# Kernel tuning notes

Hardware: AMD Instinct MI355X
Metric: run time of the kernel (lower is better)

## Reference

```python
import jax, jax.numpy as jnp
import numpy as np

N = 50000        # nodes
E = 800000       # directed edges (before self loops)
G = 1024         # graphs in batch
D = 128          # embedding_dim
H = 4            # attention heads
L = 3            # num_layers
NODE_DIM = 78
SLOPE = 0.2      # PyG GATConv leaky_relu negative slope
EPS = 1e-16


def setup_inputs() -> dict:
    key = jax.random.key(0)
    ks = jax.random.split(key, 20)
    s = lambda *sh: 1.0 / np.sqrt(sh[0])
    inp = {
        "x": jax.random.normal(ks[0], (N, NODE_DIM), jnp.float32),
        "edge_index": jax.random.randint(ks[1], (2, E), 0, N, jnp.int64),
        "batch": jnp.sort(jax.random.randint(ks[2], (N,), 0, G, jnp.int64)),
        # node_linear: Linear(78,128) -> ReLU -> Linear(128,128)
        "W1": jax.random.normal(ks[3], (NODE_DIM, D), jnp.float32) * s(NODE_DIM),
        "b1": jnp.zeros((D,), jnp.float32),
        "W2": jax.random.normal(ks[4], (D, D), jnp.float32) * s(D),
        "b2": jnp.zeros((D,), jnp.float32),
        # L stacked GATConv(D, D, heads=H, concat=False)
        "lin_w": jax.random.normal(ks[5], (L, D, H, D), jnp.float32) * s(D),
        "att_src": jax.random.normal(ks[6], (L, H, D), jnp.float32) * s(D),
        "att_dst": jax.random.normal(ks[7], (L, H, D), jnp.float32) * s(D),
        "conv_b": jnp.zeros((L, D), jnp.float32),
        # global_fc: Linear(128,1024) -> ReLU -> Dropout -> Linear(1024,128)
        "gW1": jax.random.normal(ks[8], (D, 1024), jnp.float32) * s(D),
        "gb1": jnp.zeros((1024,), jnp.float32),
        "gW2": jax.random.normal(ks[9], (1024, D), jnp.float32) * s(1024),
        "gb2": jnp.zeros((D,), jnp.float32),
    }
    return inp


def _gat_layer(x, src, dst, W, a_src, a_dst, b):
    # x: [N, D]; W: [D, H, D]
    h = jnp.einsum('nd,dhe->nhe', x, W)                    # [N, H, C]
    a_s = jnp.einsum('nhe,he->nh', h, a_src)               # [N, H]
    a_d = jnp.einsum('nhe,he->nh', h, a_dst)
    e = jax.nn.leaky_relu(a_s[src] + a_d[dst], SLOPE)      # [E', H]
    # segment softmax grouped by destination node
    m = jax.ops.segment_max(e, dst, num_segments=N)
    e = jnp.exp(e - m[dst])
    denom = jax.ops.segment_sum(e, dst, num_segments=N)
    alpha = e / (denom[dst] + EPS)                         # [E', H]
    out = jax.ops.segment_sum(h[src] * alpha[:, :, None], dst, num_segments=N)  # [N, H, C]
    return out.mean(axis=1) + b                            # concat=False: head mean


def reference(x, edge_index, batch, W1, b1, W2, b2, lin_w, att_src, att_dst,
              conv_b, gW1, gb1, gW2, gb2):
    # node_linear MLP
    h = jax.nn.relu(x @ W1 + b1) @ W2 + b2                 # [N, D]
    # add self loops (PyG GATConv default)
    loops = jnp.arange(N, dtype=edge_index.dtype)
    src = jnp.concatenate([edge_index[0], loops])
    dst = jnp.concatenate([edge_index[1], loops])
    for l in range(L):
        h = _gat_layer(h, src, dst, lin_w[l], att_src[l], att_dst[l], conv_b[l])
    # global mean pool per graph
    counts = jax.ops.segment_sum(jnp.ones((N,), h.dtype), batch, num_segments=G)
    pooled = jax.ops.segment_sum(h, batch, num_segments=G) / jnp.maximum(counts, 1.0)[:, None]
    # global_fc (dropout = identity at inference)
    return jax.nn.relu(pooled @ gW1 + gb1) @ gW2 + gb2     # [G, D]
```

## Files before the change

kernel.cpp:

```cpp
#include <hip/hip_runtime.h>
#include <hip/hip_bf16.h>

#define NN 50000
#define EE 800000
#define ET 850000
#define GG 1024
#define DD 128
#define HH 4
#define LL 3
#define ND 78
#define HD 512
#define K1P 96
#define SLOPE 0.2f
#define EPSV 1e-16f
#define SB 196
#define PADS 520

typedef __hip_bfloat16 bf16;
typedef __attribute__((ext_vector_type(8))) unsigned short u16x8;
typedef __attribute__((ext_vector_type(8))) short s16x8;
typedef __attribute__((ext_vector_type(4))) float f32x4;
typedef __attribute__((ext_vector_type(2))) float f32x2;

__device__ __forceinline__ float b2f(bf16 v) { return __bfloat162float(v); }
__device__ __forceinline__ bf16 f2b(float v) { return __float2bfloat16(v); }
__device__ __forceinline__ float bu2f(unsigned short u) {
    return __uint_as_float(((unsigned)u) << 16);
}
__device__ __forceinline__ unsigned short f2bu(float f) {
    unsigned u = __float_as_uint(f);
    unsigned rounded = u + 0x7FFFu + ((u >> 16) & 1u);
    return (unsigned short)(rounded >> 16);
}
__device__ __forceinline__ float lrelu(float e) { return (e > 0.f) ? e : SLOPE * e; }

__global__ void detect_i(const unsigned* __restrict__ w, int* __restrict__ flag) {
    __shared__ int z;
    int t = threadIdx.x;
    if (t == 0) z = 0;
    __syncthreads();
    if (w[2 * t + 1] == 0u) atomicAdd(&z, 1);
    __syncthreads();
    if (t == 0) flag[0] = (z >= 200) ? 1 : 0;
}
__global__ void conv_i(const void* __restrict__ src, int* __restrict__ dst, int n,
                       const int* __restrict__ flag) {
    int i = blockIdx.x * 256 + threadIdx.x;
    if (i >= n) return;
    const int* s = (const int*)src;
    dst[i] = flag[0] ? s[2 * i] : s[i];
}
__global__ void conv_edges(const void* __restrict__ src, int* __restrict__ dst,
                           const int* __restrict__ flag, int* __restrict__ deg) {
    int i = blockIdx.x * 256 + threadIdx.x;
    if (i < NN) deg[i] = 1;
    if (i >= 2 * EE) return;
    const int* s = (const int*)src;
    dst[i] = flag[0] ? s[2 * i] : s[i];
}

#define PRE0 (NN * K1P)
#define PRE1 (PRE0 + DD * K1P + DD * DD)
#define PRE2 (PRE1 + LL * DD * HD)
#define PRE3 (PRE2 + 2 * 1024 * DD)
#define PRE4 (PRE3 + LL * DD * HH)
#define PRE5 (PRE4 + GG * DD + GG)
__global__ void prep_misc(const float* __restrict__ x, const float* __restrict__ W1,
                          const float* __restrict__ W2, const float* __restrict__ lin_w,
                          const float* __restrict__ att_src, const float* __restrict__ att_dst,
                          const float* __restrict__ gW1, const float* __restrict__ gW2,
                          bf16* __restrict__ xb, bf16* __restrict__ W1t, bf16* __restrict__ W2t,
                          bf16* __restrict__ Bt, float* __restrict__ ws, float* __restrict__ wd,
                          bf16* __restrict__ gW1t, bf16* __restrict__ gW2t,
                          float* __restrict__ pooled, int* __restrict__ counts) {
    int idx = blockIdx.x * 256 + threadIdx.x;
    if (idx < PRE0) {
        int n = idx / K1P;
        int k = idx % K1P;
        xb[idx] = f2b((k < ND) ? x[(size_t)n * ND + k] : 0.f);
        return;
    }
    if (idx < PRE1) {
        idx -= PRE0;
        if (idx < DD * K1P) {
            int c = idx / K1P, k = idx % K1P;
            W1t[idx] = f2b((k < ND) ? W1[(size_t)k * DD + c] : 0.f);
        } else {
            idx -= DD * K1P;
            int c = idx / DD, k = idx % DD;
            W2t[idx] = f2b(W2[(size_t)k * DD + c]);
        }
        return;
    }
    if (idx < PRE2) {
        idx -= PRE1;
        int l = idx / (DD * HD);
        int rem = idx % (DD * HD);
        int c = rem / HD;
        int k = rem % HD;
        int h = k >> 7;
        int d = k & 127;
        Bt[idx] = f2b(lin_w[((size_t)(l * DD + d) * HH + h) * DD + c]);
        return;
    }
    if (idx < PRE3) {
        idx -= PRE2;
        if (idx < 1024 * DD) {
            int c = idx / DD, k = idx % DD;
            gW1t[idx] = f2b(gW1[(size_t)k * 1024 + c]);
        } else {
            idx -= 1024 * DD;
            int c = idx / 1024, k = idx % 1024;
            gW2t[idx] = f2b(gW2[(size_t)k * DD + c]);
        }
        return;
    }
    if (idx < PRE4) {
        idx -= PRE3;
        int l = idx / (DD * HH);
        int rem = idx % (DD * HH);
        int d = rem >> 2;
        int h = rem & 3;
        const float* wrow = lin_w + ((size_t)(l * DD + d) * HH + h) * DD;
        const float* as = att_src + (size_t)(l * HH + h) * DD;
        const float* ad = att_dst + (size_t)(l * HH + h) * DD;
        float s1 = 0.f, s2 = 0.f;
        for (int e = 0; e < DD; e++) { float w = wrow[e]; s1 += w * as[e]; s2 += w * ad[e]; }
        ws[idx] = s1;
        wd[idx] = s2;
        return;
    }
    if (idx < PRE5) {
        idx -= PRE4;
        if (idx < GG * DD) pooled[idx] = 0.f;
        if (idx < GG) counts[idx] = 0;
    }
}

__global__ __launch_bounds__(256) void mlp_gemm1(const bf16* __restrict__ xb,
                                                 const bf16* __restrict__ W1t,
                                                 const float* __restrict__ b1,
                                                 bf16* __restrict__ ts) {
    int wid = (blockIdx.x * 256 + threadIdx.x) >> 6;
    if (wid >= NN / 16) return;
    int lane = threadIdx.x & 63;
    int r16 = lane & 15;
    int q = lane >> 4;
    const short* ab = (const short*)xb;
    const short* bb = (const short*)W1t;
    int arow = wid * 16 + r16;
    s16x8 afr[3];
#pragma unroll
    for (int c = 0; c < 3; c++) afr[c] = *(const s16x8*)(ab + (size_t)arow * K1P + c * 32 + q * 8);
#pragma unroll
    for (int nt = 0; nt < 8; nt++) {
        int brow = nt * 16 + r16;
        f32x4 acc = {0.f, 0.f, 0.f, 0.f};
#pragma unroll
        for (int c = 0; c < 3; c++) {
            s16x8 b = *(const s16x8*)(bb + (size_t)brow * K1P + c * 32 + q * 8);
            acc = __builtin_amdgcn_mfma_f32_16x16x32_bf16(afr[c], b, acc, 0, 0, 0);
        }
        int cc = nt * 16 + r16;
        float bias = b1[cc];
#pragma unroll
        for (int r = 0; r < 4; r++) {
            int row = wid * 16 + q * 4 + r;
            ts[(size_t)row * DD + cc] = f2b(fmaxf(acc[r] + bias, 0.f));
        }
    }
}

__global__ __launch_bounds__(256) void mlp_gemm2(const bf16* __restrict__ ts,
                                                 const bf16* __restrict__ W2t,
                                                 const float* __restrict__ b2,
                                                 bf16* __restrict__ h) {
    int wid = (blockIdx.x * 256 + threadIdx.x) >> 6;
    if (wid >= NN / 16) return;
    int lane = threadIdx.x & 63;
    int r16 = lane & 15;
    int q = lane >> 4;
    const short* ab = (const short*)ts;
    const short* bb = (const short*)W2t;
    int arow = wid * 16 + r16;
    s16x8 afr[4];
#pragma unroll
    for (int c = 0; c < 4; c++) afr[c] = *(const s16x8*)(ab + (size_t)arow * DD + c * 32 + q * 8);
#pragma unroll
    for (int nt = 0; nt < 8; nt++) {
        int brow = nt * 16 + r16;
        f32x4 acc = {0.f, 0.f, 0.f, 0.f};
#pragma unroll
        for (int c = 0; c < 4; c++) {
            s16x8 b = *(const s16x8*)(bb + (size_t)brow * DD + c * 32 + q * 8);
            acc = __builtin_amdgcn_mfma_f32_16x16x32_bf16(afr[c], b, acc, 0, 0, 0);
        }
        int cc = nt * 16 + r16;
        float bias = b2[cc];
#pragma unroll
        for (int r = 0; r < 4; r++) {
            int row = wid * 16 + q * 4 + r;
            h[(size_t)row * DD + cc] = f2b(acc[r] + bias);
        }
    }
}

__global__ void hist_edges(const int* __restrict__ ei, int* deg) {
    int e = blockIdx.x * 256 + threadIdx.x;
    if (e >= EE) return;
    int dst = ei[EE + e];
    if ((unsigned)dst < NN) atomicAdd(&deg[dst], 1);
}
__global__ __launch_bounds__(256) void block_sums(const int* __restrict__ deg, int* __restrict__ bsum) {
    __shared__ int part[256];
    int t = threadIdx.x;
    int i = blockIdx.x * 256 + t;
    part[t] = (i < NN) ? deg[i] : 0;
    __syncthreads();
    for (int off = 128; off > 0; off >>= 1) {
        if (t < off) part[t] += part[t + off];
        __syncthreads();
    }
    if (t == 0) bsum[blockIdx.x] = part[0];
}
__global__ __launch_bounds__(256) void scan_bsum(const int* __restrict__ bsum, int* __restrict__ boff,
                                                 int* __restrict__ start) {
    __shared__ int part[256];
    int t = threadIdx.x;
    part[t] = (t < SB) ? bsum[t] : 0;
    __syncthreads();
    for (int off = 1; off < 256; off <<= 1) {
        int add = (t >= off) ? part[t - off] : 0;
        __syncthreads();
        part[t] += add;
        __syncthreads();
    }
    if (t < SB) boff[t] = (t == 0) ? 0 : part[t - 1];
    if (t == 255) start[NN] = part[SB - 1];
}
__global__ __launch_bounds__(256) void scan_final(const int* __restrict__ deg, const int* __restrict__ boff,
                                                  int* __restrict__ start, int* __restrict__ cursor) {
    __shared__ int part[256];
    int t = threadIdx.x;
    int i = blockIdx.x * 256 + t;
    int v = (i < NN) ? deg[i] : 0;
    part[t] = v;
    __syncthreads();
    for (int off = 1; off < 256; off <<= 1) {
        int add = (t >= off) ? part[t - off] : 0;
        __syncthreads();
        part[t] += add;
        __syncthreads();
    }
    if (i < NN) {
        int ex = boff[blockIdx.x] + part[t] - v;
        start[i] = ex;
        cursor[i] = ex;
    }
}
__global__ void scatter_all(const int* __restrict__ ei, int* cursor, int* ssrc) {
    int i = blockIdx.x * 256 + threadIdx.x;
    if (i < NN) {
        int pos = atomicAdd(&cursor[i], 1);
        if ((unsigned)pos < ET) ssrc[pos] = i;
        return;
    }
    int e = i - NN;
    if (e >= EE) return;
    int src = ei[e];
    int dst = ei[EE + e];
    if ((unsigned)dst >= NN) return;
    int pos = atomicAdd(&cursor[dst], 1);
    if ((unsigned)pos < ET) ssrc[pos] = ((unsigned)src < NN) ? src : 0;
}

__global__ __launch_bounds__(256) void a_sd2(const bf16* __restrict__ h,
                                             const float* __restrict__ ws,
                                             const float* __restrict__ wd,
                                             float* __restrict__ a_s, float* __restrict__ a_d) {
    __shared__ float wsl[DD][HH];
    __shared__ float wdl[DD][HH];
    int t = threadIdx.x;
    for (int i = t; i < DD * HH; i += 256) { wsl[i >> 2][i & 3] = ws[i]; wdl[i >> 2][i & 3] = wd[i]; }
    __syncthreads();
    int n = blockIdx.x * 256 + t;
    if (n >= NN) return;
    const u16x8* row = (const u16x8*)((const unsigned short*)h + (size_t)n * DD);
    float s1[HH] = {0.f, 0.f, 0.f, 0.f};
    float s2[HH] = {0.f, 0.f, 0.f, 0.f};
    for (int c = 0; c < 16; c++) {
        u16x8 v = row[c];
#pragma unroll
        for (int k = 0; k < 8; k++) {
            int d = c * 8 + k;
            float f = bu2f(v[k]);
#pragma unroll
            for (int hh = 0; hh < HH; hh++) {
                s1[hh] += f * wsl[d][hh];
                s2[hh] += f * wdl[d][hh];
            }
        }
    }
#pragma unroll
    for (int hh = 0; hh < HH; hh++) {
        a_s[n * HH + hh] = s1[hh];
        a_d[n * HH + hh] = s2[hh];
    }
}

__global__ __launch_bounds__(1024, 8) void agg_gemm(const int* __restrict__ start,
                                                    const int* __restrict__ ssrc,
                                                    const float* __restrict__ a_s,
                                                    const float* __restrict__ a_d,
                                                    const bf16* __restrict__ h,
                                                    const bf16* __restrict__ Bt,
                                                    const float* __restrict__ conv_b,
                                                    bf16* __restrict__ hnext) {
    __shared__ short aggL[16 * PADS];
    __shared__ float wlds[16][64][HH];
    __shared__ float mxl[16][HH];
    __shared__ float invl[16][HH];
    int wv = threadIdx.x >> 6;
    int lane = threadIdx.x & 63;
    int half = lane >> 5;
    int sl = lane & 31;
    int node16 = blockIdx.x * 16;
    int node = node16 + wv;

    int s0 = start[node];
    int deg = start[node + 1] - s0;
    int sidx = (lane < deg) ? ssrc[s0 + lane] : 0;
    int soff = sidx << 8;

    const char* hb = (const char*)h;
    int lb8 = sl << 3;

    auto issueChunk = [&](int j, uint2 (&hv)[4]) {
#pragma unroll
        for (int p = 0; p < 4; p++) {
            int sa = __builtin_amdgcn_readlane(soff, j + 2 * p);
            int sb = __builtin_amdgcn_readlane(soff, j + 2 * p + 1);
            hv[p] = *(const uint2*)(hb + ((half ? sb : sa) + lb8));
        }
    };

    int m = (deg > 64) ? 64 : deg;
    int nch = (m + 7) >> 3;
    uint2 hva[4], hvb[4];
    issueChunk(0, hva);

    {
        int jj = lane & 15;
        int hh = lane >> 4;
        float ad = a_d[node * HH + hh];
        float ec[4];
        float mx = -1e30f;
#pragma unroll
        for (int k = 0; k < 4; k++) {
            int j = jj + k * 16;
            float e = -1e30f;
            if (j < deg) {
                int s = __shfl(sidx, j);
                e = lrelu(a_s[s * HH + hh] + ad);
            }
            ec[k] = e;
            mx = fmaxf(mx, e);
        }
        for (int j = jj + 64; j < deg; j += 16) {
            int s = ssrc[s0 + j];
            mx = fmaxf(mx, lrelu(a_s[s * HH + hh] + ad));
        }
#pragma unroll
        for (int off = 1; off < 16; off <<= 1) mx = fmaxf(mx, __shfl_xor(mx, off));
        float den = 0.f;
#pragma unroll
        for (int k = 0; k < 4; k++) {
            int j = jj + k * 16;
            float ww = __expf(ec[k] - mx);
            den += ww;
            wlds[wv][j][hh] = ww;
        }
        for (int j = jj + 64; j < deg; j += 16) {
            int s = ssrc[s0 + j];
            den += __expf(lrelu(a_s[s * HH + hh] + ad) - mx);
        }
#pragma unroll
        for (int off = 1; off < 16; off <<= 1) den += __shfl_xor(den, off);
        if (jj == 0) {
            invl[wv][hh] = 1.f / (den + EPSV);
            mxl[wv][hh] = mx;
        }
    }

    f32x2 accA[HH];
    f32x2 accB[HH];
#pragma unroll
    for (int hh = 0; hh < HH; hh++) { accA[hh] = (f32x2){0.f, 0.f}; accB[hh] = (f32x2){0.f, 0.f}; }

    auto consumeChunk = [&](int j, uint2 (&hv)[4]) {
#pragma unroll
        for (int p = 0; p < 4; p++) {
            float4 w4 = *(const float4*)wlds[wv][j + 2 * p + half];
            f32x2 vA, vB;
            vA.x = __uint_as_float(hv[p].x << 16);
            vA.y = __uint_as_float(hv[p].x & 0xffff0000u);
            vB.x = __uint_as_float(hv[p].y << 16);
            vB.y = __uint_as_float(hv[p].y & 0xffff0000u);
            accA[0] += vA * w4.x; accB[0] += vB * w4.x;
            accA[1] += vA * w4.y; accB[1] += vB * w4.y;
            accA[2] += vA * w4.z; accB[2] += vB * w4.z;
            accA[3] += vA * w4.w; accB[3] += vB * w4.w;
        }
    };

    {
        int c = 0;
        for (;;) {
            if (c + 1 < nch) issueChunk((c + 1) * 8, hvb);
            consumeChunk(c * 8, hva);
            if (++c >= nch) break;
            if (c + 1 < nch) issueChunk((c + 1) * 8, hva);
            consumeChunk(c * 8, hvb);
            if (++c >= nch) break;
        }
    }

    for (int j = 64; j < deg; j++) {
        int s = ssrc[s0 + j];
        float4 as4 = *(const float4*)(a_s + (size_t)s * HH);
        float4 ad4 = *(const float4*)(a_d + (size_t)node * HH);
        float4 w4;
        float g = half ? 0.f : 1.f;
        w4.x = g * __expf(lrelu(as4.x + ad4.x) - mxl[wv][0]);
        w4.y = g * __expf(lrelu(as4.y + ad4.y) - mxl[wv][1]);
        w4.z = g * __expf(lrelu(as4.z + ad4.z) - mxl[wv][2]);
        w4.w = g * __expf(lrelu(as4.w + ad4.w) - mxl[wv][3]);
        uint2 hv = *(const uint2*)(hb + ((size_t)s << 8) + lb8);
        f32x2 vA, vB;
        vA.x = __uint_as_float(hv.x << 16);
        vA.y = __uint_as_float(hv.x & 0xffff0000u);
        vB.x = __uint_as_float(hv.y << 16);
        vB.y = __uint_as_float(hv.y & 0xffff0000u);
        accA[0] += vA * w4.x; accB[0] += vB * w4.x;
        accA[1] += vA * w4.y; accB[1] += vB * w4.y;
        accA[2] += vA * w4.z; accB[2] += vB * w4.z;
        accA[3] += vA * w4.w; accB[3] += vB * w4.w;
    }

#pragma unroll
    for (int hh = 0; hh < HH; hh++) {
        accA[hh].x += __shfl_xor(accA[hh].x, 32);
        accA[hh].y += __shfl_xor(accA[hh].y, 32);
        accB[hh].x += __shfl_xor(accB[hh].x, 32);
        accB[hh].y += __shfl_xor(accB[hh].y, 32);
    }

    float4 inv4 = *(const float4*)invl[wv];
    float invs[HH] = {inv4.x, inv4.y, inv4.z, inv4.w};
    unsigned* aggU = (unsigned*)aggL;
#pragma unroll
    for (int hh = 0; hh < HH; hh++) {
        f32x2 sel = half ? accB[hh] : accA[hh];
        unsigned packed = (unsigned)f2bu(sel.x * invs[hh]) |
                          ((unsigned)f2bu(sel.y * invs[hh]) << 16);
        aggU[wv * (PADS / 2) + hh * (DD / 2) + sl * 2 + half] = packed;
    }
    __syncthreads();

    if (wv < 8) {
        int nt = wv;
        int r16 = lane & 15;
        int q = lane >> 4;
        const short* bb = (const short*)Bt;
        int brow = nt * 16 + r16;
        f32x4 gacc = {0.f, 0.f, 0.f, 0.f};
#pragma unroll
        for (int c = 0; c < 16; c++) {
            s16x8 a = *(const s16x8*)(aggL + r16 * PADS + c * 32 + q * 8);
            s16x8 b = *(const s16x8*)(bb + (size_t)brow * HD + c * 32 + q * 8);
            gacc = __builtin_amdgcn_mfma_f32_16x16x32_bf16(a, b, gacc, 0, 0, 0);
        }
        int cc = nt * 16 + r16;
        float bias = conv_b[cc];
#pragma unroll
        for (int r = 0; r < 4; r++) {
            int row = node16 + q * 4 + r;
            hnext[(size_t)row * DD + cc] = f2b(0.25f * gacc[r] + bias);
        }
    }
}

__global__ void pool_count(const int* __restrict__ batch, int* counts) {
    int n = blockIdx.x * 256 + threadIdx.x;
    if (n >= NN) return;
    int g = batch[n];
    if ((unsigned)g < GG) atomicAdd(&counts[g], 1);
}
__global__ __launch_bounds__(256) void pool_accum2(const bf16* __restrict__ h,
                                                   const int* __restrict__ batch,
                                                   float* pooled) {
    int t = threadIdx.x;
    int d = t & 127;
    int half = t >> 7;
    int n0 = blockIdx.x * 64 + half * 32;
    int n1 = n0 + 32; if (n1 > NN) n1 = NN;
    float acc = 0.f;
    int cur = -1;
    for (int n = n0; n < n1; n++) {
        int g = batch[n];
        if ((unsigned)g >= GG) continue;
        if (g != cur) {
            if (cur >= 0) atomicAdd(&pooled[cur * DD + d], acc);
            acc = 0.f; cur = g;
        }
        acc += b2f(h[(size_t)n * DD + d]);
    }
    if (cur >= 0) atomicAdd(&pooled[cur * DD + d], acc);
}
__global__ void pooled2bf(const float* __restrict__ pooled, const int* __restrict__ counts,
                          bf16* __restrict__ pbf) {
    int idx = blockIdx.x * 256 + threadIdx.x;
    if (idx >= GG * DD) return;
    int g = idx >> 7;
    int c = counts[g]; if (c < 1) c = 1;
    pbf[idx] = f2b(pooled[idx] / (float)c);
}

__global__ __launch_bounds__(256) void fc1_mfma(const bf16* __restrict__ pbf,
                                                const bf16* __restrict__ gW1t,
                                                const float* __restrict__ gb1,
                                                bf16* __restrict__ t1) {
    int wid = (blockIdx.x * 256 + threadIdx.x) >> 6;
    int lane = threadIdx.x & 63;
    int mt = wid >> 6;
    int nt = wid & 63;
    int r16 = lane & 15;
    int q = lane >> 4;
    const short* ab = (const short*)pbf;
    const short* bb = (const short*)gW1t;
    f32x4 acc = {0.f, 0.f, 0.f, 0.f};
    int arow = mt * 16 + r16;
    int brow = nt * 16 + r16;
#pragma unroll
    for (int c = 0; c < 4; c++) {
        s16x8 a = *(const s16x8*)(ab + (size_t)arow * DD + c * 32 + q * 8);
        s16x8 b = *(const s16x8*)(bb + (size_t)brow * DD + c * 32 + q * 8);
        acc = __builtin_amdgcn_mfma_f32_16x16x32_bf16(a, b, acc, 0, 0, 0);
    }
    int cc = nt * 16 + r16;
    float bias = gb1[cc];
#pragma unroll
    for (int r = 0; r < 4; r++) {
        int row = mt * 16 + q * 4 + r;
        t1[(size_t)row * 1024 + cc] = f2b(fmaxf(acc[r] + bias, 0.f));
    }
}

__global__ __launch_bounds__(256) void fc2_mfma(const bf16* __restrict__ t1,
                                                const bf16* __restrict__ gW2t,
                                                const float* __restrict__ gb2,
                                                float* __restrict__ out) {
    int wid = (blockIdx.x * 256 + threadIdx.x) >> 6;
    int lane = threadIdx.x & 63;
    int mt = wid >> 3;
    int nt = wid & 7;
    int r16 = lane & 15;
    int q = lane >> 4;
    const short* ab = (const short*)t1;
    const short* bb = (const short*)gW2t;
    f32x4 acc = {0.f, 0.f, 0.f, 0.f};
    int arow = mt * 16 + r16;
    int brow = nt * 16 + r16;
#pragma unroll
    for (int c = 0; c < 32; c++) {
        s16x8 a = *(const s16x8*)(ab + (size_t)arow * 1024 + c * 32 + q * 8);
        s16x8 b = *(const s16x8*)(bb + (size_t)brow * 1024 + c * 32 + q * 8);
        acc = __builtin_amdgcn_mfma_f32_16x16x32_bf16(a, b, acc, 0, 0, 0);
    }
    int cc = nt * 16 + r16;
    float bias = gb2[cc];
#pragma unroll
    for (int r = 0; r < 4; r++) {
        int row = mt * 16 + q * 4 + r;
        out[(size_t)row * DD + cc] = acc[r] + bias;
    }
}

__global__ void sentinel_only(float* out, int hostcode) {
    if (threadIdx.x == 0 && blockIdx.x == 0) out[0] = (float)hostcode;
}

extern "C" void kernel_launch(void* const* d_in, const int* in_sizes, int n_in,
                              void* d_out, int out_size, void* d_ws, size_t ws_size,
                              hipStream_t stream) {
    float* out = (float*)d_out;

    static const int expect[15] = {3900000, 1600000, 50000, 9984, 128, 16384, 128,
                                   196608, 1536, 1536, 384, 131072, 1024, 131072, 128};
    int hostcode = 0;
    if (n_in != 15) hostcode = 21099;
    else for (int i = 0; i < 15; i++) if (in_sizes[i] != expect[i]) { hostcode = 21000 + i; break; }
    if (hostcode == 0 && out_size != GG * DD) hostcode = 35000;

    const float* x       = (const float*)d_in[0];
    const float* W1      = (const float*)d_in[3];
    const float* b1      = (const float*)d_in[4];
    const float* W2      = (const float*)d_in[5];
    const float* b2      = (const float*)d_in[6];
    const float* lin_w   = (const float*)d_in[7];
    const float* att_src = (const float*)d_in[8];
    const float* att_dst = (const float*)d_in[9];
    const float* conv_b  = (const float*)d_in[10];
    const float* gW1     = (const float*)d_in[11];
    const float* gb1     = (const float*)d_in[12];
    const float* gW2     = (const float*)d_in[13];
    const float* gb2     = (const float*)d_in[14];

    char* p = (char*)d_ws;
    auto alloc = [&](size_t bytes) { void* q = (void*)p; p += (bytes + 255) & ~(size_t)255; return q; };
    int*   flags  = (int*)alloc(4 * 4);
    int*   ei32   = (int*)alloc((size_t)2 * EE * 4);
    int*   bat32  = (int*)alloc((size_t)NN * 4);
    bf16*  xb     = (bf16*)alloc((size_t)NN * K1P * 2);
    bf16*  W1tb   = (bf16*)alloc((size_t)DD * K1P * 2);
    bf16*  W2tb   = (bf16*)alloc((size_t)DD * DD * 2);
    bf16*  tsbuf  = (bf16*)alloc((size_t)NN * DD * 2);
    bf16*  hA     = (bf16*)alloc((size_t)NN * DD * 2);
    bf16*  hB     = (bf16*)alloc((size_t)NN * DD * 2);
    bf16*  Bt     = (bf16*)alloc((size_t)LL * DD * HD * 2);
    float* wsbuf  = (float*)alloc((size_t)LL * DD * HH * 4);
    float* wdbuf  = (float*)alloc((size_t)LL * DD * HH * 4);
    float* a_s    = (float*)alloc((size_t)NN * HH * 4);
    float* a_d    = (float*)alloc((size_t)NN * HH * 4);
    int*   deg    = (int*)alloc((size_t)NN * 4);
    int*   start  = (int*)alloc((size_t)(NN + 1) * 4);
    int*   cursor = (int*)alloc((size_t)NN * 4);
    int*   ssrc   = (int*)alloc((size_t)ET * 4);
    int*   bsum   = (int*)alloc((size_t)SB * 4);
    int*   boff   = (int*)alloc((size_t)SB * 4);
    float* pooled = (float*)alloc((size_t)GG * DD * 4);
    int*   counts = (int*)alloc((size_t)GG * 4);
    bf16*  pbf    = (bf16*)alloc((size_t)GG * DD * 2);
    bf16*  gW1t   = (bf16*)alloc((size_t)1024 * DD * 2);
    bf16*  gW2t   = (bf16*)alloc((size_t)DD * 1024 * 2);
    bf16*  t1buf  = (bf16*)alloc((size_t)GG * 1024 * 2);
    size_t need = (size_t)(p - (char*)d_ws);
    if (hostcode == 0 && ws_size < need) hostcode = 34000;

    if (hostcode != 0) {
        sentinel_only<<<1, 64, 0, stream>>>(out, hostcode);
        return;
    }

    detect_i<<<1, 256, 0, stream>>>((const unsigned*)d_in[1], flags + 0);
    detect_i<<<1, 256, 0, stream>>>((const unsigned*)d_in[2], flags + 1);
    conv_edges<<<(2 * EE + 255) / 256, 256, 0, stream>>>(d_in[1], ei32, flags + 0, deg);
    conv_i<<<(NN + 255) / 256, 256, 0, stream>>>(d_in[2], bat32, NN, flags + 1);

    prep_misc<<<PRE5 / 256, 256, 0, stream>>>(x, W1, W2, lin_w, att_src, att_dst, gW1, gW2,
                                              xb, W1tb, W2tb, Bt, wsbuf, wdbuf, gW1t, gW2t,
                                              pooled, counts);

    mlp_gemm1<<<(NN / 16 * 64 + 255) / 256, 256, 0, stream>>>(xb, W1tb, b1, tsbuf);
    mlp_gemm2<<<(NN / 16 * 64 + 255) / 256, 256, 0, stream>>>(tsbuf, W2tb, b2, hA);

    hist_edges<<<(EE + 255) / 256, 256, 0, stream>>>(ei32, deg);
    block_sums<<<SB, 256, 0, stream>>>(deg, bsum);
    scan_bsum<<<1, 256, 0, stream>>>(bsum, boff, start);
    scan_final<<<SB, 256, 0, stream>>>(deg, boff, start, cursor);
    scatter_all<<<(NN + EE + 255) / 256, 256, 0, stream>>>(ei32, cursor, ssrc);

    bf16* hin = hA;
    bf16* hout = hB;
    for (int l = 0; l < LL; l++) {
        a_sd2<<<(NN + 255) / 256, 256, 0, stream>>>(hin, wsbuf + l * DD * HH, wdbuf + l * DD * HH, a_s, a_d);
        agg_gemm<<<NN / 16, 1024, 0, stream>>>(start, ssrc, a_s, a_d, hin,
                                               Bt + (size_t)l * DD * HD, conv_b + l * DD, hout);
        bf16* tmp = hin; hin = hout; hout = tmp;
    }
    pool_count<<<(NN + 255) / 256, 256, 0, stream>>>(bat32, counts);
    pool_accum2<<<(NN + 63) / 64, 256, 0, stream>>>(hin, bat32, pooled);
    pooled2bf<<<(GG * DD + 255) / 256, 256, 0, stream>>>(pooled, counts, pbf);
    fc1_mfma<<<(64 * 64) / 4, 256, 0, stream>>>(pbf, gW1t, gb1, t1buf);
    fc2_mfma<<<(64 * 8) / 4, 256, 0, stream>>>(t1buf, gW2t, gb2, out);
}
```

Baseline: 572.9 us.

## Fuse MLP GEMMs, attention-score epilogues, and preprocessing kernels to cut launches

Merges the two node-MLP GEMMs into one kernel that keeps the hidden tile in LDS, and computes the layer-0 attention scores in its epilogue. Each GAT aggregation kernel now also computes the next layer's a_s/a_d in its epilogue, so the separate a_sd2 pass is gone. Int64 detection, degree histogram and graph counts are folded into the conversion kernels, and the pooled normalization moves into fc1. This removes several launches and full passes over h, at the cost of extra shuffles and an extra block-wide sync in agg_gemm, plus redundant detection work repeated in every block.

```diff
diff --git a/kernel.cpp b/kernel.cpp
--- a/kernel.cpp
+++ b/kernel.cpp
@@ -34,37 +34,13 @@
 }
 __device__ __forceinline__ float lrelu(float e) { return (e > 0.f) ? e : SLOPE * e; }
 
-__global__ void detect_i(const unsigned* __restrict__ w, int* __restrict__ flag) {
-    __shared__ int z;
-    int t = threadIdx.x;
-    if (t == 0) z = 0;
-    __syncthreads();
-    if (w[2 * t + 1] == 0u) atomicAdd(&z, 1);
-    __syncthreads();
-    if (t == 0) flag[0] = (z >= 200) ? 1 : 0;
-}
-__global__ void conv_i(const void* __restrict__ src, int* __restrict__ dst, int n,
-                       const int* __restrict__ flag) {
-    int i = blockIdx.x * 256 + threadIdx.x;
-    if (i >= n) return;
-    const int* s = (const int*)src;
-    dst[i] = flag[0] ? s[2 * i] : s[i];
-}
-__global__ void conv_edges(const void* __restrict__ src, int* __restrict__ dst,
-                           const int* __restrict__ flag, int* __restrict__ deg) {
-    int i = blockIdx.x * 256 + threadIdx.x;
-    if (i < NN) deg[i] = 1;
-    if (i >= 2 * EE) return;
-    const int* s = (const int*)src;
-    dst[i] = flag[0] ? s[2 * i] : s[i];
-}
-
 #define PRE0 (NN * K1P)
 #define PRE1 (PRE0 + DD * K1P + DD * DD)
 #define PRE2 (PRE1 + LL * DD * HD)
 #define PRE3 (PRE2 + 2 * 1024 * DD)
 #define PRE4 (PRE3 + LL * DD * HH)
 #define PRE5 (PRE4 + GG * DD + GG)
+#define PRE6 (PRE5 + NN)
 __global__ void prep_misc(const float* __restrict__ x, const float* __restrict__ W1,
                           const float* __restrict__ W2, const float* __restrict__ lin_w,
                           const float* __restrict__ att_src, const float* __restrict__ att_dst,
@@ -72,7 +48,8 @@
                           bf16* __restrict__ xb, bf16* __restrict__ W1t, bf16* __restrict__ W2t,
                           bf16* __restrict__ Bt, float* __restrict__ ws, float* __restrict__ wd,
                           bf16* __restrict__ gW1t, bf16* __restrict__ gW2t,
-                          float* __restrict__ pooled, int* __restrict__ counts) {
+                          float* __restrict__ pooled, int* __restrict__ counts,
+                          int* __restrict__ deg) {
     int idx = blockIdx.x * 256 + threadIdx.x;
     if (idx < PRE0) {
         int n = idx / K1P;
@@ -134,83 +111,148 @@
         idx -= PRE4;
         if (idx < GG * DD) pooled[idx] = 0.f;
         if (idx < GG) counts[idx] = 0;
-    }
-}
-
-__global__ __launch_bounds__(256) void mlp_gemm1(const bf16* __restrict__ xb,
+        return;
+    }
+    if (idx < PRE6) {
+        deg[idx - PRE5] = 1;
+    }
+}
+
+__global__ void conv_edges(const void* __restrict__ src, int* __restrict__ dst,
+                           int* __restrict__ deg) {
+    __shared__ int z;
+    int t = threadIdx.x;
+    const unsigned* w = (const unsigned*)src;
+    if (t == 0) z = 0;
+    __syncthreads();
+    if (w[2 * t + 1] == 0u) atomicAdd(&z, 1);
+    __syncthreads();
+    int flag = (z >= 200) ? 1 : 0;
+    int i = blockIdx.x * 256 + t;
+    if (i >= 2 * EE) return;
+    const int* s = (const int*)src;
+    int g = flag ? s[2 * i] : s[i];
+    dst[i] = g;
+    if (i >= EE && (unsigned)g < NN) atomicAdd(&deg[g], 1);
+}
+
+__global__ void conv_batch(const void* __restrict__ src, int* __restrict__ dst,
+                           int* __restrict__ counts) {
+    __shared__ int z;
+    int t = threadIdx.x;
+    const unsigned* w = (const unsigned*)src;
+    if (t == 0) z = 0;
+    __syncthreads();
+    if (w[2 * t + 1] == 0u) atomicAdd(&z, 1);
+    __syncthreads();
+    int flag = (z >= 200) ? 1 : 0;
+    int i = blockIdx.x * 256 + t;
+    if (i >= NN) return;
+    const int* s = (const int*)src;
+    int g = flag ? s[2 * i] : s[i];
+    dst[i] = g;
+    if ((unsigned)g < GG) atomicAdd(&counts[g], 1);
+}
+
+__global__ __launch_bounds__(256) void mlp_fused(const bf16* __restrict__ xb,
                                                  const bf16* __restrict__ W1t,
                                                  const float* __restrict__ b1,
-                                                 bf16* __restrict__ ts) {
+                                                 const bf16* __restrict__ W2t,
+                                                 const float* __restrict__ b2,
+                                                 const float* __restrict__ ws0,
+                                                 const float* __restrict__ wd0,
+                                                 bf16* __restrict__ h,
+                                                 float* __restrict__ a_s, float* __restrict__ a_d) {
+    __shared__ __align__(16) short tsl[4][16][136];
+    int wv4 = threadIdx.x >> 6;
     int wid = (blockIdx.x * 256 + threadIdx.x) >> 6;
     if (wid >= NN / 16) return;
     int lane = threadIdx.x & 63;
     int r16 = lane & 15;
     int q = lane >> 4;
-    const short* ab = (const short*)xb;
-    const short* bb = (const short*)W1t;
-    int arow = wid * 16 + r16;
-    s16x8 afr[3];
-#pragma unroll
-    for (int c = 0; c < 3; c++) afr[c] = *(const s16x8*)(ab + (size_t)arow * K1P + c * 32 + q * 8);
-#pragma unroll
-    for (int nt = 0; nt < 8; nt++) {
-        int brow = nt * 16 + r16;
-        f32x4 acc = {0.f, 0.f, 0.f, 0.f};
-#pragma unroll
-        for (int c = 0; c < 3; c++) {
-            s16x8 b = *(const s16x8*)(bb + (size_t)brow * K1P + c * 32 + q * 8);
-            acc = __builtin_amdgcn_mfma_f32_16x16x32_bf16(afr[c], b, acc, 0, 0, 0);
-        }
-        int cc = nt * 16 + r16;
-        float bias = b1[cc];
-#pragma unroll
-        for (int r = 0; r < 4; r++) {
-            int row = wid * 16 + q * 4 + r;
-            ts[(size_t)row * DD + cc] = f2b(fmaxf(acc[r] + bias, 0.f));
-        }
-    }
-}
-
-__global__ __launch_bounds__(256) void mlp_gemm2(const bf16* __restrict__ ts,
-                                                 const bf16* __restrict__ W2t,
-                                                 const float* __restrict__ b2,
-                                                 bf16* __restrict__ h) {
-    int wid = (blockIdx.x * 256 + threadIdx.x) >> 6;
-    if (wid >= NN / 16) return;
-    int lane = threadIdx.x & 63;
-    int r16 = lane & 15;
-    int q = lane >> 4;
-    const short* ab = (const short*)ts;
-    const short* bb = (const short*)W2t;
-    int arow = wid * 16 + r16;
-    s16x8 afr[4];
-#pragma unroll
-    for (int c = 0; c < 4; c++) afr[c] = *(const s16x8*)(ab + (size_t)arow * DD + c * 32 + q * 8);
-#pragma unroll
-    for (int nt = 0; nt < 8; nt++) {
-        int brow = nt * 16 + r16;
-        f32x4 acc = {0.f, 0.f, 0.f, 0.f};
-#pragma unroll
-        for (int c = 0; c < 4; c++) {
-            s16x8 b = *(const s16x8*)(bb + (size_t)brow * DD + c * 32 + q * 8);
-            acc = __builtin_amdgcn_mfma_f32_16x16x32_bf16(afr[c], b, acc, 0, 0, 0);
-        }
-        int cc = nt * 16 + r16;
-        float bias = b2[cc];
-#pragma unroll
-        for (int r = 0; r < 4; r++) {
-            int row = wid * 16 + q * 4 + r;
-            h[(size_t)row * DD + cc] = f2b(acc[r] + bias);
-        }
-    }
-}
-
-__global__ void hist_edges(const int* __restrict__ ei, int* deg) {
-    int e = blockIdx.x * 256 + threadIdx.x;
-    if (e >= EE) return;
-    int dst = ei[EE + e];
-    if ((unsigned)dst < NN) atomicAdd(&deg[dst], 1);
-}
+
+    {
+        const short* ab = (const short*)xb;
+        const short* bb = (const short*)W1t;
+        int arow = wid * 16 + r16;
+        s16x8 afr[3];
+#pragma unroll
+        for (int c = 0; c < 3; c++) afr[c] = *(const s16x8*)(ab + (size_t)arow * K1P + c * 32 + q * 8);
+#pragma unroll
+        for (int nt = 0; nt < 8; nt++) {
+            int brow = nt * 16 + r16;
+            f32x4 acc = {0.f, 0.f, 0.f, 0.f};
+#pragma unroll
+            for (int c = 0; c < 3; c++) {
+                s16x8 b = *(const s16x8*)(bb + (size_t)brow * K1P + c * 32 + q * 8);
+                acc = __builtin_amdgcn_mfma_f32_16x16x32_bf16(afr[c], b, acc, 0, 0, 0);
+            }
+            int cc = nt * 16 + r16;
+            float bias = b1[cc];
+#pragma unroll
+            for (int r = 0; r < 4; r++)
+                tsl[wv4][q * 4 + r][cc] = (short)f2bu(fmaxf(acc[r] + bias, 0.f));
+        }
+    }
+
+    {
+        const short* bb = (const short*)W2t;
+        s16x8 afr[4];
+#pragma unroll
+        for (int c = 0; c < 4; c++)
+            afr[c] = *(const s16x8*)(&tsl[wv4][r16][c * 32 + q * 8]);
+        float part[4][8];
+#pragma unroll
+        for (int r = 0; r < 4; r++)
+#pragma unroll
+            for (int k = 0; k < 8; k++) part[r][k] = 0.f;
+#pragma unroll
+        for (int nt = 0; nt < 8; nt++) {
+            int brow = nt * 16 + r16;
+            f32x4 acc = {0.f, 0.f, 0.f, 0.f};
+#pragma unroll
+            for (int c = 0; c < 4; c++) {
+                s16x8 b = *(const s16x8*)(bb + (size_t)brow * DD + c * 32 + q * 8);
+                acc = __builtin_amdgcn_mfma_f32_16x16x32_bf16(afr[c], b, acc, 0, 0, 0);
+            }
+            int cc = nt * 16 + r16;
+            float bias = b2[cc];
+            float4 w4s = *(const float4*)(ws0 + cc * 4);
+            float4 w4d = *(const float4*)(wd0 + cc * 4);
+#pragma unroll
+            for (int r = 0; r < 4; r++) {
+                unsigned short us = f2bu(acc[r] + bias);
+                int row = wid * 16 + q * 4 + r;
+                ((unsigned short*)h)[(size_t)row * DD + cc] = us;
+                float v = bu2f(us);
+                part[r][0] += v * w4s.x; part[r][1] += v * w4s.y;
+                part[r][2] += v * w4s.z; part[r][3] += v * w4s.w;
+                part[r][4] += v * w4d.x; part[r][5] += v * w4d.y;
+                part[r][6] += v * w4d.z; part[r][7] += v * w4d.w;
+            }
+        }
+#pragma unroll
+        for (int r = 0; r < 4; r++)
+#pragma unroll
+            for (int k = 0; k < 8; k++) {
+                float v = part[r][k];
+                v += __shfl_xor(v, 1); v += __shfl_xor(v, 2);
+                v += __shfl_xor(v, 4); v += __shfl_xor(v, 8);
+                part[r][k] = v;
+            }
+        if (r16 == 0) {
+#pragma unroll
+            for (int r = 0; r < 4; r++) {
+                int row = wid * 16 + q * 4 + r;
+                *(float4*)(a_s + (size_t)row * 4) =
+                    make_float4(part[r][0], part[r][1], part[r][2], part[r][3]);
+                *(float4*)(a_d + (size_t)row * 4) =
+                    make_float4(part[r][4], part[r][5], part[r][6], part[r][7]);
+            }
+        }
+    }
+}
+
 __global__ __launch_bounds__(256) void block_sums(const int* __restrict__ deg, int* __restrict__ bsum) {
     __shared__ int part[256];
     int t = threadIdx.x;
@@ -274,40 +316,6 @@
     if ((unsigned)pos < ET) ssrc[pos] = ((unsigned)src < NN) ? src : 0;
 }
 
-__global__ __launch_bounds__(256) void a_sd2(const bf16* __restrict__ h,
-                                             const float* __restrict__ ws,
-                                             const float* __restrict__ wd,
-                                             float* __restrict__ a_s, float* __restrict__ a_d) {
-    __shared__ float wsl[DD][HH];
-    __shared__ float wdl[DD][HH];
-    int t = threadIdx.x;
-    for (int i = t; i < DD * HH; i += 256) { wsl[i >> 2][i & 3] = ws[i]; wdl[i >> 2][i & 3] = wd[i]; }
-    __syncthreads();
-    int n = blockIdx.x * 256 + t;
-    if (n >= NN) return;
-    const u16x8* row = (const u16x8*)((const unsigned short*)h + (size_t)n * DD);
-    float s1[HH] = {0.f, 0.f, 0.f, 0.f};
-    float s2[HH] = {0.f, 0.f, 0.f, 0.f};
-    for (int c = 0; c < 16; c++) {
-        u16x8 v = row[c];
-#pragma unroll
-        for (int k = 0; k < 8; k++) {
-            int d = c * 8 + k;
-            float f = bu2f(v[k]);
-#pragma unroll
-            for (int hh = 0; hh < HH; hh++) {
-                s1[hh] += f * wsl[d][hh];
-                s2[hh] += f * wdl[d][hh];
-            }
-        }
-    }
-#pragma unroll
-    for (int hh = 0; hh < HH; hh++) {
-        a_s[n * HH + hh] = s1[hh];
-        a_d[n * HH + hh] = s2[hh];
-    }
-}
-
 __global__ __launch_bounds__(1024, 8) void agg_gemm(const int* __restrict__ start,
                                                     const int* __restrict__ ssrc,
                                                     const float* __restrict__ a_s,
@@ -315,11 +323,17 @@
                                                     const bf16* __restrict__ h,
                                                     const bf16* __restrict__ Bt,
                                                     const float* __restrict__ conv_b,
-                                                    bf16* __restrict__ hnext) {
+                                                    bf16* __restrict__ hnext,
+                                                    const float* __restrict__ wsn,
+                                                    const float* __restrict__ wdn,
+                                                    float* __restrict__ a_s_out,
+                                                    float* __restrict__ a_d_out,
+                                                    int has_next) {
     __shared__ short aggL[16 * PADS];
     __shared__ float wlds[16][64][HH];
     __shared__ float mxl[16][HH];
     __shared__ float invl[16][HH];
+    __shared__ float asd_p[8][16][8];
     int wv = threadIdx.x >> 6;
     int lane = threadIdx.x & 63;
     int half = lane >> 5;
@@ -482,20 +496,54 @@
         }
         int cc = nt * 16 + r16;
         float bias = conv_b[cc];
+        float4 w4s = {0.f, 0.f, 0.f, 0.f}, w4d = {0.f, 0.f, 0.f, 0.f};
+        if (has_next) {
+            w4s = *(const float4*)(wsn + cc * 4);
+            w4d = *(const float4*)(wdn + cc * 4);
+        }
+        float pp[4][8];
 #pragma unroll
         for (int r = 0; r < 4; r++) {
+            unsigned short us = f2bu(0.25f * gacc[r] + bias);
             int row = node16 + q * 4 + r;
-            hnext[(size_t)row * DD + cc] = f2b(0.25f * gacc[r] + bias);
-        }
-    }
-}
-
-__global__ void pool_count(const int* __restrict__ batch, int* counts) {
-    int n = blockIdx.x * 256 + threadIdx.x;
-    if (n >= NN) return;
-    int g = batch[n];
-    if ((unsigned)g < GG) atomicAdd(&counts[g], 1);
-}
+            ((unsigned short*)hnext)[(size_t)row * DD + cc] = us;
+            float v = bu2f(us);
+            pp[r][0] = v * w4s.x; pp[r][1] = v * w4s.y; pp[r][2] = v * w4s.z; pp[r][3] = v * w4s.w;
+            pp[r][4] = v * w4d.x; pp[r][5] = v * w4d.y; pp[r][6] = v * w4d.z; pp[r][7] = v * w4d.w;
+        }
+        if (has_next) {
+#pragma unroll
+            for (int r = 0; r < 4; r++)
+#pragma unroll
+                for (int k = 0; k < 8; k++) {
+                    float v = pp[r][k];
+                    v += __shfl_xor(v, 1); v += __shfl_xor(v, 2);
+                    v += __shfl_xor(v, 4); v += __shfl_xor(v, 8);
+                    pp[r][k] = v;
+                }
+            if (r16 == 0) {
+#pragma unroll
+                for (int r = 0; r < 4; r++)
+#pragma unroll
+                    for (int k = 0; k < 8; k++) asd_p[wv][q * 4 + r][k] = pp[r][k];
+            }
+        }
+    }
+    if (has_next) {
+        __syncthreads();
+        int t = threadIdx.x;
+        if (t < 128) {
+            int row = t >> 3, k = t & 7;
+            float s = 0.f;
+#pragma unroll
+            for (int n2 = 0; n2 < 8; n2++) s += asd_p[n2][row][k];
+            int grow = node16 + row;
+            if (k < 4) a_s_out[grow * 4 + k] = s;
+            else       a_d_out[grow * 4 + (k - 4)] = s;
+        }
+    }
+}
+
 __global__ __launch_bounds__(256) void pool_accum2(const bf16* __restrict__ h,
                                                    const int* __restrict__ batch,
                                                    float* pooled) {
@@ -517,16 +565,9 @@
     }
     if (cur >= 0) atomicAdd(&pooled[cur * DD + d], acc);
 }
-__global__ void pooled2bf(const float* __restrict__ pooled, const int* __restrict__ counts,
-                          bf16* __restrict__ pbf) {
-    int idx = blockIdx.x * 256 + threadIdx.x;
-    if (idx >= GG * DD) return;
-    int g = idx >> 7;
-    int c = counts[g]; if (c < 1) c = 1;
-    pbf[idx] = f2b(pooled[idx] / (float)c);
-}
-
-__global__ __launch_bounds__(256) void fc1_mfma(const bf16* __restrict__ pbf,
+
+__global__ __launch_bounds__(256) void fc1_mfma(const float* __restrict__ pooled,
+                                                const int* __restrict__ counts,
                                                 const bf16* __restrict__ gW1t,
                                                 const float* __restrict__ gb1,
                                                 bf16* __restrict__ t1) {
@@ -536,14 +577,22 @@
     int nt = wid & 63;
     int r16 = lane & 15;
     int q = lane >> 4;
-    const short* ab = (const short*)pbf;
+    int arow = mt * 16 + r16;
+    int c0 = counts[arow]; if (c0 < 1) c0 = 1;
+    float inv = 1.f / (float)c0;
     const short* bb = (const short*)gW1t;
     f32x4 acc = {0.f, 0.f, 0.f, 0.f};
-    int arow = mt * 16 + r16;
     int brow = nt * 16 + r16;
 #pragma unroll
     for (int c = 0; c < 4; c++) {
-        s16x8 a = *(const s16x8*)(ab + (size_t)arow * DD + c * 32 + q * 8);
+        const float* pr = pooled + (size_t)arow * DD + c * 32 + q * 8;
+        float4 f0 = *(const float4*)pr;
+        float4 f1 = *(const float4*)(pr + 4);
+        s16x8 a;
+        a[0] = (short)f2bu(f0.x * inv); a[1] = (short)f2bu(f0.y * inv);
+        a[2] = (short)f2bu(f0.z * inv); a[3] = (short)f2bu(f0.w * inv);
+        a[4] = (short)f2bu(f1.x * inv); a[5] = (short)f2bu(f1.y * inv);
+        a[6] = (short)f2bu(f1.z * inv); a[7] = (short)f2bu(f1.w * inv);
         s16x8 b = *(const s16x8*)(bb + (size_t)brow * DD + c * 32 + q * 8);
         acc = __builtin_amdgcn_mfma_f32_16x16x32_bf16(a, b, acc, 0, 0, 0);
     }
@@ -618,20 +667,20 @@
 
     char* p = (char*)d_ws;
     auto alloc = [&](size_t bytes) { void* q = (void*)p; p += (bytes + 255) & ~(size_t)255; return q; };
-    int*   flags  = (int*)alloc(4 * 4);
     int*   ei32   = (int*)alloc((size_t)2 * EE * 4);
     int*   bat32  = (int*)alloc((size_t)NN * 4);
     bf16*  xb     = (bf16*)alloc((size_t)NN * K1P * 2);
     bf16*  W1tb   = (bf16*)alloc((size_t)DD * K1P * 2);
     bf16*  W2tb   = (bf16*)alloc((size_t)DD * DD * 2);
-    bf16*  tsbuf  = (bf16*)alloc((size_t)NN * DD * 2);
     bf16*  hA     = (bf16*)alloc((size_t)NN * DD * 2);
     bf16*  hB     = (bf16*)alloc((size_t)NN * DD * 2);
     bf16*  Bt     = (bf16*)alloc((size_t)LL * DD * HD * 2);
     float* wsbuf  = (float*)alloc((size_t)LL * DD * HH * 4);
     float* wdbuf  = (float*)alloc((size_t)LL * DD * HH * 4);
-    float* a_s    = (float*)alloc((size_t)NN * HH * 4);
-    float* a_d    = (float*)alloc((size_t)NN * HH * 4);
+    float* a_sA   = (float*)alloc((size_t)NN * HH * 4);
+    float* a_dA   = (float*)alloc((size_t)NN * HH * 4);
+    float* a_sB   = (float*)alloc((size_t)NN * HH * 4);
+    float* a_dB   = (float*)alloc((size_t)NN * HH * 4);
     int*   deg    = (int*)alloc((size_t)NN * 4);
     int*   start  = (int*)alloc((size_t)(NN + 1) * 4);
     int*   cursor = (int*)alloc((size_t)NN * 4);
@@ -640,7 +689,6 @@
     int*   boff   = (int*)alloc((size_t)SB * 4);
     float* pooled = (float*)alloc((size_t)GG * DD * 4);
     int*   counts = (int*)alloc((size_t)GG * 4);
-    bf16*  pbf    = (bf16*)alloc((size_t)GG * DD * 2);
     bf16*  gW1t   = (bf16*)alloc((size_t)1024 * DD * 2);
     bf16*  gW2t   = (bf16*)alloc((size_t)DD * 1024 * 2);
     bf16*  t1buf  = (bf16*)alloc((size_t)GG * 1024 * 2);
@@ -652,19 +700,15 @@
         return;
     }
 
-    detect_i<<<1, 256, 0, stream>>>((const unsigned*)d_in[1], flags + 0);
-    detect_i<<<1, 256, 0, stream>>>((const unsigned*)d_in[2], flags + 1);
-    conv_edges<<<(2 * EE + 255) / 256, 256, 0, stream>>>(d_in[1], ei32, flags + 0, deg);
-    conv_i<<<(NN + 255) / 256, 256, 0, stream>>>(d_in[2], bat32, NN, flags + 1);
-
-    prep_misc<<<PRE5 / 256, 256, 0, stream>>>(x, W1, W2, lin_w, att_src, att_dst, gW1, gW2,
-                                              xb, W1tb, W2tb, Bt, wsbuf, wdbuf, gW1t, gW2t,
-                                              pooled, counts);
-
-    mlp_gemm1<<<(NN / 16 * 64 + 255) / 256, 256, 0, stream>>>(xb, W1tb, b1, tsbuf);
-    mlp_gemm2<<<(NN / 16 * 64 + 255) / 256, 256, 0, stream>>>(tsbuf, W2tb, b2, hA);
-
-    hist_edges<<<(EE + 255) / 256, 256, 0, stream>>>(ei32, deg);
+    prep_misc<<<(PRE6 + 255) / 256, 256, 0, stream>>>(x, W1, W2, lin_w, att_src, att_dst, gW1, gW2,
+                                                      xb, W1tb, W2tb, Bt, wsbuf, wdbuf, gW1t, gW2t,
+                                                      pooled, counts, deg);
+    conv_edges<<<(2 * EE + 255) / 256, 256, 0, stream>>>(d_in[1], ei32, deg);
+    conv_batch<<<(NN + 255) / 256, 256, 0, stream>>>(d_in[2], bat32, counts);
+
+    mlp_fused<<<(NN / 16 * 64 + 255) / 256, 256, 0, stream>>>(xb, W1tb, b1, W2tb, b2,
+                                                              wsbuf, wdbuf, hA, a_sA, a_dA);
+
     block_sums<<<SB, 256, 0, stream>>>(deg, bsum);
     scan_bsum<<<1, 256, 0, stream>>>(bsum, boff, start);
     scan_final<<<SB, 256, 0, stream>>>(deg, boff, start, cursor);
@@ -672,15 +716,20 @@
 
     bf16* hin = hA;
     bf16* hout = hB;
+    float* asin = a_sA; float* adin = a_dA;
+    float* asout = a_sB; float* adout = a_dB;
     for (int l = 0; l < LL; l++) {
-        a_sd2<<<(NN + 255) / 256, 256, 0, stream>>>(hin, wsbuf + l * DD * HH, wdbuf + l * DD * HH, a_s, a_d);
-        agg_gemm<<<NN / 16, 1024, 0, stream>>>(start, ssrc, a_s, a_d, hin,
-                                               Bt + (size_t)l * DD * HD, conv_b + l * DD, hout);
+        int has = (l < LL - 1) ? 1 : 0;
+        const float* wsn = has ? (wsbuf + (size_t)(l + 1) * DD * HH) : wsbuf;
+        const float* wdn = has ? (wdbuf + (size_t)(l + 1) * DD * HH) : wdbuf;
+        agg_gemm<<<NN / 16, 1024, 0, stream>>>(start, ssrc, asin, adin, hin,
+                                               Bt + (size_t)l * DD * HD, conv_b + l * DD, hout,
+                                               wsn, wdn, asout, adout, has);
         bf16* tmp = hin; hin = hout; hout = tmp;
-    }
-    pool_count<<<(NN + 255) / 256, 256, 0, stream>>>(bat32, counts);
+        float* t1 = asin; asin = asout; asout = t1;
+        float* t2 = adin; adin = adout; adout = t2;
+    }
     pool_accum2<<<(NN + 63) / 64, 256, 0, stream>>>(hin, bat32, pooled);
-    pooled2bf<<<(GG * DD + 255) / 256, 256, 0, stream>>>(pooled, counts, pbf);
-    fc1_mfma<<<(64 * 64) / 4, 256, 0, stream>>>(pbf, gW1t, gb1, t1buf);
+    fc1_mfma<<<(64 * 64) / 4, 256, 0, stream>>>(pooled, counts, gW1t, gb1, t1buf);
     fc2_mfma<<<(64 * 8) / 4, 256, 0, stream>>>(t1buf, gW2t, gb2, out);
 }
```

New measurement: 588.4 us. 1.03x slower.
